# Optimization experiments

Hardware: AMD Instinct MI355X
Metric: run time of the kernel (lower is better)

The kernel has to match this reference:

```python
import jax, jax.numpy as jnp
import numpy as np

EPS = 1e-5

def _bn(x, gamma, beta):
    # training-mode BatchNorm1d over (batch, length) per channel; x: [B, C, N]
    mean = x.mean(axis=(0, 2), keepdims=True)
    var = x.var(axis=(0, 2), keepdims=True)
    return (x - mean) * jax.lax.rsqrt(var + EPS) * gamma[None, :, None] + beta[None, :, None]

def setup_inputs() -> dict:
    key = jax.random.key(0)
    ks = jax.random.split(key, 16)
    B, N = 8, 4096
    def w(k, o, i):
        return jax.random.normal(k, (o, i), jnp.float32) * (1.0 / np.sqrt(i))
    return {
        "x": jax.random.normal(ks[0], (B, 3, N), jnp.float32),
        "w_mlp1": w(ks[1], 64, 3),
        "g1": jax.random.uniform(ks[2], (64,), jnp.float32, 0.5, 1.5),
        "b1": jax.random.normal(ks[3], (64,), jnp.float32) * 0.1,
        "w_mlp2": w(ks[4], 128, 64),
        "wq": w(ks[5], 16, 128),
        "g2": jax.random.uniform(ks[6], (16,), jnp.float32, 0.5, 1.5),
        "b2": jax.random.normal(ks[7], (16,), jnp.float32) * 0.1,
        "wk": w(ks[8], 16, 128),
        "g3": jax.random.uniform(ks[9], (16,), jnp.float32, 0.5, 1.5),
        "b3": jax.random.normal(ks[10], (16,), jnp.float32) * 0.1,
        "wv": w(ks[11], 3, 128),
        "g4": jax.random.uniform(ks[12], (3,), jnp.float32, 0.5, 1.5),
        "b4": jax.random.normal(ks[13], (3,), jnp.float32) * 0.1,
        "alpha": jax.random.uniform(ks[14], (1,), jnp.float32, 0.1, 1.0),
    }

def reference(x, w_mlp1, g1, b1, w_mlp2, wq, g2, b2, wk, g3, b3, wv, g4, b4, alpha):
    # mlp: conv1(k=1) -> BN -> LeakyReLU(0.2) -> conv1(k=1)
    h = jnp.einsum('oc,bcn->bon', w_mlp1, x)                       # [B,64,N]
    h = jax.nn.leaky_relu(_bn(h, g1, b1), negative_slope=0.2)
    feat = jnp.einsum('oc,bcn->bon', w_mlp2, h)                    # [B,128,N]
    q = jax.nn.relu(_bn(jnp.einsum('oc,bcn->bon', wq, feat), g2, b2))  # [B,16,N]
    k = jax.nn.relu(_bn(jnp.einsum('oc,bcn->bon', wk, feat), g3, b3))  # [B,16,N]
    v = jax.nn.relu(_bn(jnp.einsum('oc,bcn->bon', wv, feat), g4, b4))  # [B,3,N]
    # similarity = softmax(K^T Q) over last dim (no scale, as in source)
    sim = jax.nn.softmax(jnp.einsum('bdn,bdm->bnm', k, q), axis=-1)    # [B,N,N]
    # out = V @ sim^T
    out = jnp.einsum('bcm,bnm->bcn', v, sim)                           # [B,3,N]
    return alpha[0] * out + x
```

## Files before the change

kernel.cpp:

```cpp
#include <hip/hip_runtime.h>

#define EPS 1e-5f
constexpr int NN = 4096;
constexpr float INV_CNT = 1.0f / (8.0f * 4096.0f);
constexpr float LOG2E = 1.44269504f;

typedef __attribute__((ext_vector_type(8))) short bf16x8;
typedef __attribute__((ext_vector_type(4))) float f32x4;
typedef __attribute__((ext_vector_type(4))) _Float16 f16x4;
typedef __fp16 fp16x2 __attribute__((ext_vector_type(2)));

#if __has_builtin(__builtin_amdgcn_exp2f)
#define EXP2F(x) __builtin_amdgcn_exp2f(x)
#else
#define EXP2F(x) exp2f(x)
#endif

constexpr size_t OFF_QPT = 0;
constexpr size_t OFF_KPT = 524288;
constexpr size_t OFF_VPT = 1048576;
constexpr size_t OFF_WT2 = 1179648;
constexpr size_t OFF_XP  = 1181952;
constexpr size_t OFF_BS  = 1183104;
constexpr size_t OFF_QH  = 1201024;
constexpr size_t OFF_QL  = 1463168;
constexpr size_t OFF_KH  = 1725312;
constexpr size_t OFF_KL  = 1987456;
constexpr size_t OFF_VFH = 2249600;
constexpr size_t OFF_PL  = 2315136;
constexpr size_t OFF_PA0 = 2446208;
constexpr size_t OFF_PA1 = 2577280;
constexpr size_t OFF_PA2 = 2708352;
constexpr size_t OFF_PM  = 2839424;

__global__ __launch_bounds__(256) void kA_mom_wcomb(
    const float* __restrict__ x, float* __restrict__ xpart,
    const float* __restrict__ w2, const float* __restrict__ wq,
    const float* __restrict__ wk, const float* __restrict__ wv,
    float* __restrict__ wt2) {
  __shared__ float w2s[8192];
  __shared__ float wr[4480];
  __shared__ float sred[36];
  int tx = threadIdx.x;
  if (blockIdx.x < 128) {
    int idx = blockIdx.x * 256 + tx;
    int b = idx >> 12, n = idx & 4095;
    float x0 = x[(size_t)(b*3+0)*NN + n];
    float x1 = x[(size_t)(b*3+1)*NN + n];
    float x2 = x[(size_t)(b*3+2)*NN + n];
    float m[9] = {x0, x1, x2, x0*x0, x0*x1, x0*x2, x1*x1, x1*x2, x2*x2};
    #pragma unroll
    for (int off = 32; off; off >>= 1) {
      #pragma unroll
      for (int j = 0; j < 9; ++j) m[j] += __shfl_xor(m[j], off);
    }
    int w = tx >> 6;
    if ((tx & 63) == 0) {
      #pragma unroll
      for (int j = 0; j < 9; ++j) sred[w*9+j] = m[j];
    }
    __syncthreads();
    if (tx < 9) xpart[tx*128 + blockIdx.x] = sred[tx] + sred[9+tx] + sred[18+tx] + sred[27+tx];
  } else {
    for (int i = tx; i < 8192; i += 256) w2s[i] = w2[i];
    for (int i = tx; i < 2048; i += 256) { wr[i] = wq[i]; wr[2048+i] = wk[i]; }
    for (int i = tx; i < 384; i += 256) wr[4096+i] = wv[i];
    __syncthreads();
    for (int e = tx; e < 2240; e += 256) {
      int j = e >> 6, c = e & 63;
      float s = 0.f;
      #pragma unroll 4
      for (int o = 0; o < 128; ++o) s = fmaf(wr[j*128+o], w2s[o*64+c], s);
      wt2[c*36 + j] = s;
    }
  }
}

__global__ __launch_bounds__(128) void kB_qkv(
    const float* __restrict__ x, const float* __restrict__ xpart,
    const float* __restrict__ w1, const float* __restrict__ g1,
    const float* __restrict__ b1, const float* __restrict__ wt2,
    float* __restrict__ qpT, float* __restrict__ kpT, float* __restrict__ vpT,
    float* __restrict__ bs) {
  __shared__ float4 w1s[64];
  __shared__ float4 wt2s[576];
  __shared__ float sred[140];
  __shared__ float mom[9];
  int tx = threadIdx.x;
  for (int i = tx; i < 576; i += 128) wt2s[i] = ((const float4*)wt2)[i];
  if (tx < 9) {
    float acc = 0.f;
    #pragma unroll 8
    for (int i = 0; i < 128; ++i) acc += xpart[tx*128 + i];
    mom[tx] = acc * INV_CNT;
  }
  __syncthreads();
  if (tx < 64) {
    int c = tx;
    float a = w1[c*3], b_ = w1[c*3+1], d = w1[c*3+2];
    float mean = a*mom[0] + b_*mom[1] + d*mom[2];
    float e2 = a*a*mom[3] + b_*b_*mom[6] + d*d*mom[8]
             + 2.f*(a*b_*mom[4] + a*d*mom[5] + b_*d*mom[7]);
    float sc = g1[c] * rsqrtf(e2 - mean*mean + EPS);
    w1s[c] = make_float4(a*sc, b_*sc, d*sc, fmaf(-mean, sc, b1[c]));
  }
  __syncthreads();
  int idx = blockIdx.x*128 + tx;
  int b = idx >> 12, n = idx & 4095;
  float x0 = x[(size_t)(b*3+0)*NN + n];
  float x1 = x[(size_t)(b*3+1)*NN + n];
  float x2 = x[(size_t)(b*3+2)*NN + n];
  float qa[16] = {}, ka[16] = {};
  float va0 = 0.f, va1 = 0.f, va2 = 0.f;
  #pragma unroll 4
  for (int c = 0; c < 64; ++c) {
    float4 w = w1s[c];
    float h = fmaf(w.x, x0, fmaf(w.y, x1, fmaf(w.z, x2, w.w)));
    h = h > 0.f ? h : 0.2f*h;
    #pragma unroll
    for (int j = 0; j < 4; ++j) {
      float4 A = wt2s[c*9 + j];
      qa[4*j+0] = fmaf(A.x, h, qa[4*j+0]);
      qa[4*j+1] = fmaf(A.y, h, qa[4*j+1]);
      qa[4*j+2] = fmaf(A.z, h, qa[4*j+2]);
      qa[4*j+3] = fmaf(A.w, h, qa[4*j+3]);
      float4 B = wt2s[c*9 + 4 + j];
      ka[4*j+0] = fmaf(B.x, h, ka[4*j+0]);
      ka[4*j+1] = fmaf(B.y, h, ka[4*j+1]);
      ka[4*j+2] = fmaf(B.z, h, ka[4*j+2]);
      ka[4*j+3] = fmaf(B.w, h, ka[4*j+3]);
    }
    float4 V = wt2s[c*9 + 8];
    va0 = fmaf(V.x, h, va0); va1 = fmaf(V.y, h, va1); va2 = fmaf(V.z, h, va2);
  }
  float4* qo = (float4*)(qpT + (size_t)idx*16);
  float4* ko = (float4*)(kpT + (size_t)idx*16);
  #pragma unroll
  for (int j = 0; j < 4; ++j) {
    qo[j] = make_float4(qa[4*j], qa[4*j+1], qa[4*j+2], qa[4*j+3]);
    ko[j] = make_float4(ka[4*j], ka[4*j+1], ka[4*j+2], ka[4*j+3]);
  }
  ((float4*)vpT)[idx] = make_float4(va0, va1, va2, 0.f);
  int w = tx >> 6;
  bool lead = ((tx & 63) == 0);
  #pragma unroll
  for (int d = 0; d < 16; ++d) {
    float s = qa[d], q = qa[d]*qa[d];
    #pragma unroll
    for (int off = 32; off; off >>= 1) { s += __shfl_xor(s, off); q += __shfl_xor(q, off); }
    if (lead) { sred[w*70 + d] = s; sred[w*70 + 16 + d] = q; }
    s = ka[d]; q = ka[d]*ka[d];
    #pragma unroll
    for (int off = 32; off; off >>= 1) { s += __shfl_xor(s, off); q += __shfl_xor(q, off); }
    if (lead) { sred[w*70 + 32 + d] = s; sred[w*70 + 48 + d] = q; }
  }
  float vv[3] = {va0, va1, va2};
  #pragma unroll
  for (int d = 0; d < 3; ++d) {
    float s = vv[d], q = vv[d]*vv[d];
    #pragma unroll
    for (int off = 32; off; off >>= 1) { s += __shfl_xor(s, off); q += __shfl_xor(q, off); }
    if (lead) { sred[w*70 + 64 + d] = s; sred[w*70 + 67 + d] = q; }
  }
  __syncthreads();
  if (tx < 70)
    bs[tx*256 + blockIdx.x] = sred[tx] + sred[70+tx];
}

__global__ __launch_bounds__(256) void kC_prep(
    const float* __restrict__ qpT, const float* __restrict__ kpT,
    const float* __restrict__ vpT, const float* __restrict__ bs,
    const float* __restrict__ g2, const float* __restrict__ b2,
    const float* __restrict__ g3, const float* __restrict__ b3,
    const float* __restrict__ g4, const float* __restrict__ b4,
    uint4* __restrict__ qh, uint4* __restrict__ ql,
    uint4* __restrict__ kh, uint4* __restrict__ kl,
    _Float16* __restrict__ vfh) {
  __shared__ float tot[70];
  __shared__ float spr[70];
  int tx = threadIdx.x;
  if (tx < 70) {
    float acc = 0.f;
    #pragma unroll 8
    for (int i = 0; i < 256; ++i) acc += bs[tx*256 + i];
    tot[tx] = acc * INV_CNT;
  }
  __syncthreads();
  if (tx < 16) {
    float mean = tot[tx], var = tot[16+tx] - mean*mean;
    float sc = g2[tx]*rsqrtf(var + EPS);
    spr[tx] = sc * LOG2E;
    spr[16+tx] = fmaf(-mean, sc, b2[tx]) * LOG2E;
  } else if (tx < 32) {
    int d = tx-16;
    float mean = tot[32+d], var = tot[48+d] - mean*mean;
    float sc = g3[d]*rsqrtf(var + EPS);
    spr[32+d] = sc; spr[48+d] = fmaf(-mean, sc, b3[d]);
  } else if (tx < 35) {
    int d = tx-32;
    float mean = tot[64+d], var = tot[67+d] - mean*mean;
    float sc = g4[d]*rsqrtf(var + EPS);
    spr[64+d] = sc; spr[67+d] = fmaf(-mean, sc, b4[d]);
  }
  __syncthreads();
  int p = blockIdx.x*256 + tx;
  float qv[16], kv[16];
  const float4* q4 = (const float4*)(qpT + (size_t)p*16);
  const float4* k4p = (const float4*)(kpT + (size_t)p*16);
  #pragma unroll
  for (int j = 0; j < 4; ++j) {
    float4 tq = q4[j], tk = k4p[j];
    qv[4*j] = tq.x; qv[4*j+1] = tq.y; qv[4*j+2] = tq.z; qv[4*j+3] = tq.w;
    kv[4*j] = tk.x; kv[4*j+1] = tk.y; kv[4*j+2] = tk.z; kv[4*j+3] = tk.w;
  }
  #pragma unroll
  for (int d = 0; d < 16; ++d) {
    qv[d] = fmaxf(fmaf(qv[d], spr[d],    spr[16+d]), 0.f);
    kv[d] = fmaxf(fmaf(kv[d], spr[32+d], spr[48+d]), 0.f);
  }
  unsigned qhw[8], qlw[8], khw[8], klw[8];
  #pragma unroll
  for (int j = 0; j < 8; ++j) {
    unsigned u0 = __float_as_uint(qv[2*j]),   u1 = __float_as_uint(qv[2*j+1]);
    unsigned h0 = u0 & 0xFFFF0000u, h1 = u1 & 0xFFFF0000u;
    float l0 = qv[2*j] - __uint_as_float(h0);
    float l1 = qv[2*j+1] - __uint_as_float(h1);
    qhw[j] = (h0 >> 16) | h1;
    qlw[j] = (__float_as_uint(l0) >> 16) | (__float_as_uint(l1) & 0xFFFF0000u);
    u0 = __float_as_uint(kv[2*j]); u1 = __float_as_uint(kv[2*j+1]);
    h0 = u0 & 0xFFFF0000u; h1 = u1 & 0xFFFF0000u;
    l0 = kv[2*j] - __uint_as_float(h0);
    l1 = kv[2*j+1] - __uint_as_float(h1);
    khw[j] = (h0 >> 16) | h1;
    klw[j] = (__float_as_uint(l0) >> 16) | (__float_as_uint(l1) & 0xFFFF0000u);
  }
  qh[(size_t)p*2+0] = make_uint4(qhw[0], qhw[1], qhw[2], qhw[3]);
  qh[(size_t)p*2+1] = make_uint4(qhw[4], qhw[5], qhw[6], qhw[7]);
  ql[(size_t)p*2+0] = make_uint4(qlw[0], qlw[1], qlw[2], qlw[3]);
  ql[(size_t)p*2+1] = make_uint4(qlw[4], qlw[5], qlw[6], qlw[7]);
  kh[(size_t)p*2+0] = make_uint4(khw[0], khw[1], khw[2], khw[3]);
  kh[(size_t)p*2+1] = make_uint4(khw[4], khw[5], khw[6], khw[7]);
  kl[(size_t)p*2+0] = make_uint4(klw[0], klw[1], klw[2], klw[3]);
  kl[(size_t)p*2+1] = make_uint4(klw[4], klw[5], klw[6], klw[7]);
  float4 vv = ((const float4*)vpT)[p];
  vfh[0*32768 + p] = (_Float16)fmaxf(fmaf(vv.x, spr[64], spr[67]), 0.f);
  vfh[1*32768 + p] = (_Float16)fmaxf(fmaf(vv.y, spr[65], spr[68]), 0.f);
  vfh[2*32768 + p] = (_Float16)fmaxf(fmaf(vv.z, spr[66], spr[69]), 0.f);
  vfh[3*32768 + p] = (_Float16)1.0f;
}

__global__ __launch_bounds__(128, 8) void k5_attn(
    const uint4* __restrict__ qh, const uint4* __restrict__ ql,
    const uint4* __restrict__ kh, const uint4* __restrict__ kl,
    const _Float16* __restrict__ vfh,
    float* __restrict__ pm, float* __restrict__ pl, float* __restrict__ pa0,
    float* __restrict__ pa1, float* __restrict__ pa2) {
  int tx = threadIdx.x;
  int cb = blockIdx.x & 3;
  int rb = blockIdx.x >> 2;
  int b  = rb >> 7;
  int rc = rb & 127;
  int w = tx >> 6, lane = tx & 63;
  int nl = lane & 15, g = lane >> 4, g1 = g & 1;
  int n0 = rc*32 + w*16;
  size_t pbase = (size_t)b*4096;
  size_t kp2 = (pbase + n0 + nl)*2;
  bf16x8 bKh = *(const bf16x8*)&kh[kp2 + g1];
  bf16x8 bKl = *(const bf16x8*)&kl[kp2 + g1];
  f32x4 zero4 = {0.f, 0.f, 0.f, 0.f};
  f32x4 acc = {0.f, 0.f, 0.f, 0.f};
  float M = 0.f;
  size_t cbase = pbase + (size_t)cb*1024;
  const uint4* qptr = ((g < 2) ? qh : ql) + (cbase + nl)*2 + g1;
  const _Float16* vptr = vfh + (size_t)nl*32768 + cbase + g*4;
  bool vload = (nl < 4);
  f16x4 zeroh = {(_Float16)0.f, (_Float16)0.f, (_Float16)0.f, (_Float16)0.f};
  #pragma unroll 4
  for (int ct = 0; ct < 64; ++ct) {
    bf16x8 aQ = *(const bf16x8*)qptr;
    qptr += 32;
    f32x4 c = __builtin_amdgcn_mfma_f32_16x16x32_bf16(aQ, bKh, zero4, 0, 0, 0);
    c = __builtin_amdgcn_mfma_f32_16x16x32_bf16(aQ, bKl, c, 0, 0, 0);
    float cmax = fmaxf(fmaxf(c[0], c[1]), fmaxf(c[2], c[3]));
    cmax = fmaxf(cmax, __shfl_xor(cmax, 16));
    cmax = fmaxf(cmax, __shfl_xor(cmax, 32));
    float Mn = fmaxf(M, cmax);
    float cc = EXP2F(M - Mn);
    acc[0] *= cc; acc[1] *= cc; acc[2] *= cc; acc[3] *= cc;
    M = Mn;
    union { fp16x2 h2[2]; f16x4 v4; } pw;
    pw.h2[0] = __builtin_amdgcn_cvt_pkrtz(EXP2F(c[0] - M), EXP2F(c[1] - M));
    pw.h2[1] = __builtin_amdgcn_cvt_pkrtz(EXP2F(c[2] - M), EXP2F(c[3] - M));
    f16x4 av = zeroh;
    if (vload) av = *(const f16x4*)vptr;
    vptr += 16;
    acc = __builtin_amdgcn_mfma_f32_16x16x16f16(av, pw.v4, acc, 0, 0, 0);
  }
  if (lane < 16) {
    size_t base = (size_t)cb*32768 + pbase + n0 + lane;
    pm[base] = M; pl[base] = acc[3];
    pa0[base] = acc[0]; pa1[base] = acc[1]; pa2[base] = acc[2];
  }
}

__global__ __launch_bounds__(256) void k6_merge(
    const float* __restrict__ pm, const float* __restrict__ pl,
    const float* __restrict__ pa0, const float* __restrict__ pa1,
    const float* __restrict__ pa2, const float* __restrict__ x,
    const float* __restrict__ alpha, float* __restrict__ out) {
  int row = blockIdx.x*256 + threadIdx.x;
  float m0 = pm[row],           m1 = pm[32768+row];
  float m2 = pm[2*32768+row],   m3 = pm[3*32768+row];
  float M = fmaxf(fmaxf(m0, m1), fmaxf(m2, m3));
  float c0 = exp2f(m0 - M), c1 = exp2f(m1 - M);
  float c2 = exp2f(m2 - M), c3 = exp2f(m3 - M);
  float L  = pl[row]*c0  + pl[32768+row]*c1  + pl[2*32768+row]*c2  + pl[3*32768+row]*c3;
  float A0 = pa0[row]*c0 + pa0[32768+row]*c1 + pa0[2*32768+row]*c2 + pa0[3*32768+row]*c3;
  float A1 = pa1[row]*c0 + pa1[32768+row]*c1 + pa1[2*32768+row]*c2 + pa1[3*32768+row]*c3;
  float A2 = pa2[row]*c0 + pa2[32768+row]*c1 + pa2[2*32768+row]*c2 + pa2[3*32768+row]*c3;
  int b = row >> 12, n = row & 4095;
  float inv = 1.f / L, al = alpha[0];
  out[(size_t)(b*3+0)*NN + n] = fmaf(al, A0*inv, x[(size_t)(b*3+0)*NN + n]);
  out[(size_t)(b*3+1)*NN + n] = fmaf(al, A1*inv, x[(size_t)(b*3+1)*NN + n]);
  out[(size_t)(b*3+2)*NN + n] = fmaf(al, A2*inv, x[(size_t)(b*3+2)*NN + n]);
}

extern "C" void kernel_launch(void* const* d_in, const int* in_sizes, int n_in,
                              void* d_out, int out_size, void* d_ws, size_t ws_size,
                              hipStream_t stream) {
  const float* x    = (const float*)d_in[0];
  const float* w1   = (const float*)d_in[1];
  const float* g1   = (const float*)d_in[2];
  const float* b1   = (const float*)d_in[3];
  const float* w2   = (const float*)d_in[4];
  const float* wq   = (const float*)d_in[5];
  const float* g2   = (const float*)d_in[6];
  const float* b2   = (const float*)d_in[7];
  const float* wk   = (const float*)d_in[8];
  const float* g3   = (const float*)d_in[9];
  const float* b3   = (const float*)d_in[10];
  const float* wv   = (const float*)d_in[11];
  const float* g4   = (const float*)d_in[12];
  const float* b4   = (const float*)d_in[13];
  const float* alpha= (const float*)d_in[14];
  float* out = (float*)d_out;
  float* ws  = (float*)d_ws;

  float* qpT = ws + OFF_QPT;
  float* kpT = ws + OFF_KPT;
  float* vpT = ws + OFF_VPT;
  float* wt2 = ws + OFF_WT2;
  float* xp  = ws + OFF_XP;
  float* bst = ws + OFF_BS;
  uint4* qhb = (uint4*)(ws + OFF_QH);
  uint4* qlb = (uint4*)(ws + OFF_QL);
  uint4* khb = (uint4*)(ws + OFF_KH);
  uint4* klb = (uint4*)(ws + OFF_KL);
  _Float16* vfh = (_Float16*)(ws + OFF_VFH);
  float* pls = ws + OFF_PL;
  float* pa0 = ws + OFF_PA0;
  float* pa1 = ws + OFF_PA1;
  float* pa2 = ws + OFF_PA2;
  float* pms = ws + OFF_PM;

  kA_mom_wcomb<<<129, 256, 0, stream>>>(x, xp, w2, wq, wk, wv, wt2);
  kB_qkv<<<256, 128, 0, stream>>>(x, xp, w1, g1, b1, wt2, qpT, kpT, vpT, bst);
  kC_prep<<<128, 256, 0, stream>>>(qpT, kpT, vpT, bst, g2, b2, g3, b3, g4, b4,
                                   qhb, qlb, khb, klb, vfh);
  k5_attn<<<4096, 128, 0, stream>>>(qhb, qlb, khb, klb, vfh, pms, pls, pa0, pa1, pa2);
  k6_merge<<<128, 256, 0, stream>>>(pms, pls, pa0, pa1, pa2, x, alpha, out);
}
```

Before: 101.7 us.

## Precompute softmax row max in separate pass, drop online rescaling

New measurement: 155.7 us. +53.1%, slower.

```diff
diff --git a/kernel.cpp b/kernel.cpp
--- a/kernel.cpp
+++ b/kernel.cpp
@@ -7,6 +7,7 @@
 
 typedef __attribute__((ext_vector_type(8))) short bf16x8;
 typedef __attribute__((ext_vector_type(4))) float f32x4;
+typedef __attribute__((ext_vector_type(16))) float f32x16;
 typedef __attribute__((ext_vector_type(4))) _Float16 f16x4;
 typedef __fp16 fp16x2 __attribute__((ext_vector_type(2)));
 
@@ -27,11 +28,11 @@
 constexpr size_t OFF_KH  = 1725312;
 constexpr size_t OFF_KL  = 1987456;
 constexpr size_t OFF_VFH = 2249600;
-constexpr size_t OFF_PL  = 2315136;
-constexpr size_t OFF_PA0 = 2446208;
-constexpr size_t OFF_PA1 = 2577280;
-constexpr size_t OFF_PA2 = 2708352;
-constexpr size_t OFF_PM  = 2839424;
+constexpr size_t OFF_PL  = 2511744;
+constexpr size_t OFF_PA0 = 2642816;
+constexpr size_t OFF_PA1 = 2773888;
+constexpr size_t OFF_PA2 = 2904960;
+constexpr size_t OFF_PMX = 3036032;
 
 __global__ __launch_bounds__(256) void kA_mom_wcomb(
     const float* __restrict__ x, float* __restrict__ xpart,
@@ -249,11 +250,47 @@
   vfh[3*32768 + p] = (_Float16)1.0f;
 }
 
-__global__ __launch_bounds__(128, 8) void k5_attn(
+__global__ __launch_bounds__(256, 4) void k5max(
+    const uint4* __restrict__ qh, const uint4* __restrict__ kh,
+    float* __restrict__ pmax) {
+  int tx = threadIdx.x;
+  int b  = blockIdx.x >> 5;
+  int rc = blockIdx.x & 31;
+  int w = tx >> 6, lane = tx & 63;
+  int cl = lane & 31, hl = lane >> 5;
+  int n0 = rc*128 + w*32;
+  size_t pbase = (size_t)b*4096;
+  bf16x8 aK = *(const bf16x8*)&kh[(pbase + n0 + cl)*2 + hl];
+  f32x16 zero16;
+  #pragma unroll
+  for (int r = 0; r < 16; ++r) zero16[r] = 0.f;
+  f32x16 lm = zero16;
+  const uint4* qptr = &qh[(pbase + cl)*2 + hl];
+  #pragma unroll 2
+  for (int ct = 0; ct < 128; ++ct) {
+    bf16x8 bQ = *(const bf16x8*)qptr;
+    qptr += 64;
+    f32x16 c = __builtin_amdgcn_mfma_f32_32x32x16_bf16(aK, bQ, zero16, 0, 0, 0);
+    #pragma unroll
+    for (int r = 0; r < 16; ++r) lm[r] = fmaxf(lm[r], c[r]);
+  }
+  #pragma unroll
+  for (int off = 1; off <= 16; off <<= 1) {
+    #pragma unroll
+    for (int r = 0; r < 16; ++r) lm[r] = fmaxf(lm[r], __shfl_xor(lm[r], off));
+  }
+  if (cl == 0) {
+    #pragma unroll
+    for (int r = 0; r < 16; ++r)
+      pmax[pbase + n0 + (r & 3) + 8*(r >> 2) + 4*hl] = lm[r];
+  }
+}
+
+__global__ __launch_bounds__(128, 8) void k5pv(
     const uint4* __restrict__ qh, const uint4* __restrict__ ql,
     const uint4* __restrict__ kh, const uint4* __restrict__ kl,
-    const _Float16* __restrict__ vfh,
-    float* __restrict__ pm, float* __restrict__ pl, float* __restrict__ pa0,
+    const _Float16* __restrict__ vfh, const float* __restrict__ pmax,
+    float* __restrict__ pl, float* __restrict__ pa0,
     float* __restrict__ pa1, float* __restrict__ pa2) {
   int tx = threadIdx.x;
   int cb = blockIdx.x & 3;
@@ -267,57 +304,42 @@
   size_t kp2 = (pbase + n0 + nl)*2;
   bf16x8 bKh = *(const bf16x8*)&kh[kp2 + g1];
   bf16x8 bKl = *(const bf16x8*)&kl[kp2 + g1];
+  float Mrow = pmax[pbase + n0 + nl];
   f32x4 zero4 = {0.f, 0.f, 0.f, 0.f};
   f32x4 acc = {0.f, 0.f, 0.f, 0.f};
-  float M = 0.f;
   size_t cbase = pbase + (size_t)cb*1024;
   const uint4* qptr = ((g < 2) ? qh : ql) + (cbase + nl)*2 + g1;
   const _Float16* vptr = vfh + (size_t)nl*32768 + cbase + g*4;
-  bool vload = (nl < 4);
-  f16x4 zeroh = {(_Float16)0.f, (_Float16)0.f, (_Float16)0.f, (_Float16)0.f};
   #pragma unroll 4
   for (int ct = 0; ct < 64; ++ct) {
     bf16x8 aQ = *(const bf16x8*)qptr;
     qptr += 32;
     f32x4 c = __builtin_amdgcn_mfma_f32_16x16x32_bf16(aQ, bKh, zero4, 0, 0, 0);
     c = __builtin_amdgcn_mfma_f32_16x16x32_bf16(aQ, bKl, c, 0, 0, 0);
-    float cmax = fmaxf(fmaxf(c[0], c[1]), fmaxf(c[2], c[3]));
-    cmax = fmaxf(cmax, __shfl_xor(cmax, 16));
-    cmax = fmaxf(cmax, __shfl_xor(cmax, 32));
-    float Mn = fmaxf(M, cmax);
-    float cc = EXP2F(M - Mn);
-    acc[0] *= cc; acc[1] *= cc; acc[2] *= cc; acc[3] *= cc;
-    M = Mn;
     union { fp16x2 h2[2]; f16x4 v4; } pw;
-    pw.h2[0] = __builtin_amdgcn_cvt_pkrtz(EXP2F(c[0] - M), EXP2F(c[1] - M));
-    pw.h2[1] = __builtin_amdgcn_cvt_pkrtz(EXP2F(c[2] - M), EXP2F(c[3] - M));
-    f16x4 av = zeroh;
-    if (vload) av = *(const f16x4*)vptr;
+    pw.h2[0] = __builtin_amdgcn_cvt_pkrtz(EXP2F(c[0] - Mrow), EXP2F(c[1] - Mrow));
+    pw.h2[1] = __builtin_amdgcn_cvt_pkrtz(EXP2F(c[2] - Mrow), EXP2F(c[3] - Mrow));
+    f16x4 av = *(const f16x4*)vptr;
     vptr += 16;
     acc = __builtin_amdgcn_mfma_f32_16x16x16f16(av, pw.v4, acc, 0, 0, 0);
   }
   if (lane < 16) {
     size_t base = (size_t)cb*32768 + pbase + n0 + lane;
-    pm[base] = M; pl[base] = acc[3];
+    pl[base] = acc[3];
     pa0[base] = acc[0]; pa1[base] = acc[1]; pa2[base] = acc[2];
   }
 }
 
 __global__ __launch_bounds__(256) void k6_merge(
-    const float* __restrict__ pm, const float* __restrict__ pl,
-    const float* __restrict__ pa0, const float* __restrict__ pa1,
-    const float* __restrict__ pa2, const float* __restrict__ x,
-    const float* __restrict__ alpha, float* __restrict__ out) {
+    const float* __restrict__ pl, const float* __restrict__ pa0,
+    const float* __restrict__ pa1, const float* __restrict__ pa2,
+    const float* __restrict__ x, const float* __restrict__ alpha,
+    float* __restrict__ out) {
   int row = blockIdx.x*256 + threadIdx.x;
-  float m0 = pm[row],           m1 = pm[32768+row];
-  float m2 = pm[2*32768+row],   m3 = pm[3*32768+row];
-  float M = fmaxf(fmaxf(m0, m1), fmaxf(m2, m3));
-  float c0 = exp2f(m0 - M), c1 = exp2f(m1 - M);
-  float c2 = exp2f(m2 - M), c3 = exp2f(m3 - M);
-  float L  = pl[row]*c0  + pl[32768+row]*c1  + pl[2*32768+row]*c2  + pl[3*32768+row]*c3;
-  float A0 = pa0[row]*c0 + pa0[32768+row]*c1 + pa0[2*32768+row]*c2 + pa0[3*32768+row]*c3;
-  float A1 = pa1[row]*c0 + pa1[32768+row]*c1 + pa1[2*32768+row]*c2 + pa1[3*32768+row]*c3;
-  float A2 = pa2[row]*c0 + pa2[32768+row]*c1 + pa2[2*32768+row]*c2 + pa2[3*32768+row]*c3;
+  float L  = pl[row]  + pl[32768+row]  + pl[2*32768+row]  + pl[3*32768+row];
+  float A0 = pa0[row] + pa0[32768+row] + pa0[2*32768+row] + pa0[3*32768+row];
+  float A1 = pa1[row] + pa1[32768+row] + pa1[2*32768+row] + pa1[3*32768+row];
+  float A2 = pa2[row] + pa2[32768+row] + pa2[2*32768+row] + pa2[3*32768+row];
   int b = row >> 12, n = row & 4095;
   float inv = 1.f / L, al = alpha[0];
   out[(size_t)(b*3+0)*NN + n] = fmaf(al, A0*inv, x[(size_t)(b*3+0)*NN + n]);
@@ -361,12 +383,13 @@
   float* pa0 = ws + OFF_PA0;
   float* pa1 = ws + OFF_PA1;
   float* pa2 = ws + OFF_PA2;
-  float* pms = ws + OFF_PM;
+  float* pmx = ws + OFF_PMX;
 
   kA_mom_wcomb<<<129, 256, 0, stream>>>(x, xp, w2, wq, wk, wv, wt2);
   kB_qkv<<<256, 128, 0, stream>>>(x, xp, w1, g1, b1, wt2, qpT, kpT, vpT, bst);
   kC_prep<<<128, 256, 0, stream>>>(qpT, kpT, vpT, bst, g2, b2, g3, b3, g4, b4,
                                    qhb, qlb, khb, klb, vfh);
-  k5_attn<<<4096, 128, 0, stream>>>(qhb, qlb, khb, klb, vfh, pms, pls, pa0, pa1, pa2);
-  k6_merge<<<128, 256, 0, stream>>>(pms, pls, pa0, pa1, pa2, x, alpha, out);
-}
+  k5max<<<256, 256, 0, stream>>>(qhb, khb, pmx);
+  k5pv<<<4096, 128, 0, stream>>>(qhb, qlb, khb, klb, vfh, pmx, pls, pa0, pa1, pa2);
+  k6_merge<<<128, 256, 0, stream>>>(pls, pa0, pa1, pa2, x, alpha, out);
+}
```
